# Performance work log

Measured on AMD Instinct MI355X. Metric: run time of the kernel, lower is better.

Reference implementation:

```python
import jax, jax.numpy as jnp
import numpy as np
import math

NUM_HEADS = 16


def _alibi_slopes(n):
    # n is a power of 2 here (16)
    start = 2.0 ** (-2.0 ** (-(math.log2(n) - 3)))
    return jnp.asarray([start * (start ** i) for i in range(n)], dtype=jnp.float32)


def setup_inputs() -> dict:
    key = jax.random.key(0)
    ks = jax.random.split(key, 7)
    B, S, D = 2, 2048, 1024
    s = 0.02
    return {
        "query": jax.random.normal(ks[0], (B, S, D), jnp.float32),
        "key": jax.random.normal(ks[1], (B, S, D), jnp.float32),
        "value": jax.random.normal(ks[2], (B, S, D), jnp.float32),
        "Wq": jax.random.normal(ks[3], (D, D), jnp.float32) * s,
        "Wk": jax.random.normal(ks[4], (D, D), jnp.float32) * s,
        "Wv": jax.random.normal(ks[5], (D, D), jnp.float32) * s,
        "Wo": jax.random.normal(ks[6], (D, D), jnp.float32) * s,
    }


def reference(query, key, value, Wq, Wk, Wv, Wo):
    B, S, D = query.shape
    H = NUM_HEADS
    hd = D // H
    scale = math.sqrt(hd)

    # projections (bias-free linears), split into heads: [B, S, H, hd]
    Q = (query @ Wq).reshape(B, S, H, hd)
    K = (key @ Wk).reshape(B, -1, H, hd)
    V = (value @ Wv).reshape(B, -1, H, hd)

    # attention scores [B, H, S, S]
    scores = jnp.einsum("bqhd,bkhd->bhqk", Q, K) / scale

    # ALiBi bias: -slope_h * |i - j|, broadcast over batch
    pos = jnp.arange(S, dtype=jnp.float32)
    rel = jnp.abs(pos[None, :] - pos[:, None])  # [S, S]
    slopes = _alibi_slopes(H)
    scores = scores - slopes[None, :, None, None] * rel[None, None, :, :]

    attn = jax.nn.softmax(scores, axis=-1)
    out = jnp.einsum("bhqk,bkhd->bqhd", attn, V).reshape(B, S, D)
    return out @ Wo
```

## Files before the change

kernel.cpp:

```cpp
#include <hip/hip_runtime.h>
#include <cstdint>
#include <cstddef>


typedef unsigned short u16;
typedef __attribute__((ext_vector_type(8))) _Float16 half8;
typedef __attribute__((ext_vector_type(4))) float f32x4;

#define DEVI static __device__ __forceinline__
#define MFMA16(a, b, c) __builtin_amdgcn_mfma_f32_16x16x32_f16(a, b, c, 0, 0, 0)

DEVI u16 f2h_bits(float f) {
  _Float16 h = (_Float16)f;
  union { _Float16 h; u16 u; } v; v.h = h;
  return v.u;
}

DEVI void gl_lds16(const u16* g, u16* l) {
  __builtin_amdgcn_global_load_lds(
      (const __attribute__((address_space(1))) void*)g,
      (__attribute__((address_space(3))) void*)l, 16, 0, 0);
}

__global__ __launch_bounds__(256) void cast3_h(const float* __restrict__ in0,
                                               const float* __restrict__ in1,
                                               const float* __restrict__ in2,
                                               u16* __restrict__ o0,
                                               u16* __restrict__ o1,
                                               u16* __restrict__ o2, int n) {
  const float* in = blockIdx.z == 0 ? in0 : (blockIdx.z == 1 ? in1 : in2);
  u16* out = blockIdx.z == 0 ? o0 : (blockIdx.z == 1 ? o1 : o2);
  int i = (blockIdx.x * 256 + threadIdx.x) * 4;
  if (i + 3 < n) {
    const float4 v = *(const float4*)(in + i);
    ushort4 o;
    o.x = f2h_bits(v.x); o.y = f2h_bits(v.y); o.z = f2h_bits(v.z); o.w = f2h_bits(v.w);
    *(ushort4*)(out + i) = o;
  }
}

__global__ __launch_bounds__(256) void transpose4_h(
    const float* __restrict__ W0, const float* __restrict__ W1,
    const float* __restrict__ W2, const float* __restrict__ W3,
    u16* __restrict__ T0, u16* __restrict__ T1, u16* __restrict__ T2,
    u16* __restrict__ T3) {
  const float* W = blockIdx.z == 0 ? W0 : (blockIdx.z == 1 ? W1 : (blockIdx.z == 2 ? W2 : W3));
  u16* Wt = blockIdx.z == 0 ? T0 : (blockIdx.z == 1 ? T1 : (blockIdx.z == 2 ? T2 : T3));
  __shared__ float tile[32][33];
  const int bx = blockIdx.x * 32;
  const int by = blockIdx.y * 32;
  const int x = threadIdx.x & 31;
  const int y0 = threadIdx.x >> 5;
#pragma unroll
  for (int i = y0; i < 32; i += 8)
    tile[i][x] = W[(size_t)(by + i) * 1024 + bx + x];
  __syncthreads();
#pragma unroll
  for (int i = y0; i < 32; i += 8)
    Wt[(size_t)(bx + i) * 1024 + by + x] = f2h_bits(tile[x][i]);
}

DEVI void gemm_body(const u16* __restrict__ A, const u16* __restrict__ Bt,
                    void* __restrict__ Cout, int mode, u16* As, u16* Bs) {
  constexpr int K = 1024, N = 1024;
  const int t = threadIdx.x;
  const int lane = t & 63;
  const int quad = lane >> 4;
  const int l16 = lane & 15;
  const int wid = t >> 6;
  const int mBase = blockIdx.y * 128;
  const int nBase = blockIdx.x * 128;
  const int wM = (wid >> 1) * 64;
  const int wN = (wid & 1) * 64;
  const int aswz = (quad ^ ((l16 >> 1) & 3)) << 3;

  f32x4 acc[4][4];
#pragma unroll
  for (int i = 0; i < 4; ++i)
#pragma unroll
    for (int j = 0; j < 4; ++j) acc[i][j] = (f32x4){0.f, 0.f, 0.f, 0.f};

  for (int kt = 0; kt < K / 32; ++kt) {
    const int kB = kt * 32;
    __syncthreads();
#pragma unroll
    for (int i = 0; i < 2; ++i) {
      const int ci = i * 256 + t;
      const int row = ci >> 2;
      const int col = (((ci & 3) ^ ((ci >> 3) & 3)) << 3);
      gl_lds16(A + (size_t)(mBase + row) * K + kB + col, As + ci * 8);
      gl_lds16(Bt + (size_t)(nBase + row) * K + kB + col, Bs + ci * 8);
    }
    __syncthreads();

    half8 a[4], b[4];
#pragma unroll
    for (int mi = 0; mi < 4; ++mi)
      a[mi] = *(const half8*)(As + (wM + mi * 16 + l16) * 32 + aswz);
#pragma unroll
    for (int ni = 0; ni < 4; ++ni)
      b[ni] = *(const half8*)(Bs + (wN + ni * 16 + l16) * 32 + aswz);
#pragma unroll
    for (int mi = 0; mi < 4; ++mi)
#pragma unroll
      for (int ni = 0; ni < 4; ++ni)
        acc[mi][ni] = MFMA16(a[mi], b[ni], acc[mi][ni]);
  }

#pragma unroll
  for (int mi = 0; mi < 4; ++mi) {
#pragma unroll
    for (int ni = 0; ni < 4; ++ni) {
#pragma unroll
      for (int r = 0; r < 4; ++r) {
        const int m = mBase + wM + mi * 16 + quad * 4 + r;
        const int n = nBase + wN + ni * 16 + l16;
        const float v = acc[mi][ni][r];
        if (mode == 0) {
          ((float*)Cout)[(size_t)m * N + n] = v;
        } else if (mode == 1) {
          ((u16*)Cout)[(size_t)m * N + n] = f2h_bits(v);
        } else {
          ((u16*)Cout)[(((size_t)(m >> 11) * 1024 + n) << 11) | (size_t)(m & 2047)] = f2h_bits(v);
        }
      }
    }
  }
}

__global__ __launch_bounds__(256) void proj_qkv(
    const u16* __restrict__ qb, const u16* __restrict__ kb, const u16* __restrict__ vb,
    const u16* __restrict__ Wqt, const u16* __restrict__ Wkt, const u16* __restrict__ Wvt,
    u16* __restrict__ Qp, u16* __restrict__ Kp, u16* __restrict__ Vtp) {
  __shared__ u16 As[128 * 32];
  __shared__ u16 Bs[128 * 32];
  const int z = blockIdx.z;
  const u16* A = z == 0 ? qb : (z == 1 ? kb : vb);
  const u16* Bt = z == 0 ? Wqt : (z == 1 ? Wkt : Wvt);
  void* C = z == 0 ? (void*)Qp : (z == 1 ? (void*)Kp : (void*)Vtp);
  gemm_body(A, Bt, C, z == 2 ? 2 : 1, As, Bs);
}

__global__ __launch_bounds__(256) void gemm_out(const u16* __restrict__ Ao,
                                                const u16* __restrict__ Wot,
                                                float* __restrict__ out) {
  __shared__ u16 As[128 * 32];
  __shared__ u16 Bs[128 * 32];
  gemm_body(Ao, Wot, out, 0, As, Bs);
}

__global__ __launch_bounds__(256, 4) void flash_alibi(
    const u16* __restrict__ Qg, const u16* __restrict__ Kg,
    const u16* __restrict__ Vtg, u16* __restrict__ Og) {
  constexpr int S = 2048, Dm = 1024, HD = 64;
  __shared__ u16 Ks[2][64 * 64];
  __shared__ u16 Vs[2][64 * 64];
  __shared__ u16 Ps[64 * 64];
  const int t = threadIdx.x, lane = t & 63, wid = t >> 6;
  const int quad = lane >> 4, l16 = lane & 15;
  const int qt = blockIdx.x, b = blockIdx.z;
  const int h = 15 - blockIdx.y;
  const int qBase = qt * 64;
  const size_t qRow0 = (size_t)b * S + qBase;
  const float sl2 = __builtin_amdgcn_exp2f(-0.5f * (float)(h + 1)) * 1.44269504f;
  const float sc2 = 0.125f * 1.44269504f;
  const int Di = (int)(30.0f / sl2);
  const int ktLo = max(0, (qBase - Di) >> 6);
  const int ktHi = min(31, (qBase + 63 + Di) >> 6);
  const int cswz = ((l16 & 7) << 3);
  const int pRowBase = wid * 16;

#pragma unroll
  for (int i = 0; i < 2; ++i) {
    const int ci = i * 256 + t;
    const int row = ci >> 3, col = (((ci & 7) ^ (row & 7)) << 3);
    gl_lds16(Qg + (qRow0 + row) * Dm + h * HD + col, Ps + ci * 8);
  }
  {
    const int kB = ktLo * 64;
#pragma unroll
    for (int i = 0; i < 2; ++i) {
      const int ci = i * 256 + t;
      const int row = ci >> 3, col = (((ci & 7) ^ (row & 7)) << 3);
      gl_lds16(Kg + ((size_t)b * S + kB + row) * Dm + h * HD + col, Ks[0] + ci * 8);
      gl_lds16(Vtg + ((size_t)(b * 16 + h) * HD + row) * S + kB + col, Vs[0] + ci * 8);
    }
  }

  float bi[4];
#pragma unroll
  for (int r = 0; r < 4; ++r)
    bi[r] = sl2 * (float)(qBase + wid * 16 + quad * 4 + r);

  f32x4 acc_o[4];
#pragma unroll
  for (int nd = 0; nd < 4; ++nd) acc_o[nd] = (f32x4){0.f, 0.f, 0.f, 0.f};
  float lrow[4] = {0.f, 0.f, 0.f, 0.f};

  __syncthreads();

  half8 aq[2];
#pragma unroll
  for (int ks = 0; ks < 2; ++ks) {
    const int ck = ((ks * 4 + quad) << 3) ^ cswz;
    aq[ks] = *(const half8*)(Ps + (pRowBase + l16) * HD + ck);
  }

  int bb = 0;
  for (int kt = ktLo; kt <= ktHi; ++kt) {
    const int kB = kt * 64;
    if (kt < ktHi) {
      const int kBn = kB + 64;
#pragma unroll
      for (int i = 0; i < 2; ++i) {
        const int ci = i * 256 + t;
        const int row = ci >> 3, col = (((ci & 7) ^ (row & 7)) << 3);
        gl_lds16(Kg + ((size_t)b * S + kBn + row) * Dm + h * HD + col, Ks[bb ^ 1] + ci * 8);
        gl_lds16(Vtg + ((size_t)(b * 16 + h) * HD + row) * S + kBn + col, Vs[bb ^ 1] + ci * 8);
      }
    }

    const u16* Kb = Ks[bb];
    const u16* Vb = Vs[bb];

    f32x4 s4[4];
#pragma unroll
    for (int ni = 0; ni < 4; ++ni) s4[ni] = (f32x4){0.f, 0.f, 0.f, 0.f};
    __builtin_amdgcn_s_setprio(1);
#pragma unroll
    for (int ks = 0; ks < 2; ++ks) {
      const int ck = ((ks * 4 + quad) << 3) ^ cswz;
#pragma unroll
      for (int ni = 0; ni < 4; ++ni) {
        const half8 bk = *(const half8*)(Kb + (ni * 16 + l16) * HD + ck);
        s4[ni] = MFMA16(aq[ks], bk, s4[ni]);
      }
    }
    __builtin_amdgcn_s_setprio(0);

    float bj[4];
#pragma unroll
    for (int ni = 0; ni < 4; ++ni) bj[ni] = sl2 * (float)(kB + ni * 16 + l16);
#pragma unroll
    for (int r = 0; r < 4; ++r) {
      float rs = 0.f;
      const int prow = (pRowBase + quad * 4 + r) * 64;
#pragma unroll
      for (int ni = 0; ni < 4; ++ni) {
        const float d = fabsf(bi[r] - bj[ni]);
        const float p = __builtin_amdgcn_exp2f(s4[ni][r] * sc2 - d);
        rs += p;
        Ps[prow + ((ni * 16 + l16) ^ (quad << 4))] = f2h_bits(p);
      }
      lrow[r] += rs;
    }
    __asm__ volatile("s_waitcnt lgkmcnt(0)" ::: "memory");

    __builtin_amdgcn_s_setprio(1);
#pragma unroll
    for (int ks = 0; ks < 2; ++ks) {
      const int pk = (ks * 32 + quad * 8) ^ ((l16 & 12) << 2);
      const int ck = ((ks * 4 + quad) << 3) ^ cswz;
      const half8 aP = *(const half8*)(Ps + (pRowBase + l16) * 64 + pk);
#pragma unroll
      for (int nd = 0; nd < 4; ++nd) {
        const half8 bv = *(const half8*)(Vb + (nd * 16 + l16) * HD + ck);
        acc_o[nd] = MFMA16(aP, bv, acc_o[nd]);
      }
    }
    __builtin_amdgcn_s_setprio(0);

    __syncthreads();
    bb ^= 1;
  }

#pragma unroll
  for (int r = 0; r < 4; ++r) {
    float l = lrow[r];
    l += __shfl_xor(l, 1);
    l += __shfl_xor(l, 2);
    l += __shfl_xor(l, 4);
    l += __shfl_xor(l, 8);
    const float inv = 1.f / l;
    const int rloc = wid * 16 + quad * 4 + r;
#pragma unroll
    for (int nd = 0; nd < 4; ++nd)
      Og[(qRow0 + rloc) * Dm + h * HD + nd * 16 + l16] = f2h_bits(acc_o[nd][r] * inv);
  }
}

extern "C" void kernel_launch(void* const* d_in, const int* in_sizes, int n_in,
                              void* d_out, int out_size, void* d_ws, size_t ws_size,
                              hipStream_t stream) {
  const float* q  = (const float*)d_in[0];
  const float* k  = (const float*)d_in[1];
  const float* v  = (const float*)d_in[2];
  const float* Wq = (const float*)d_in[3];
  const float* Wk = (const float*)d_in[4];
  const float* Wv = (const float*)d_in[5];
  const float* Wo = (const float*)d_in[6];
  char* ws = (char*)d_ws;
  const size_t MB = 1ull << 20;
  u16* qb  = (u16*)(ws + 0 * MB);
  u16* kb  = (u16*)(ws + 8 * MB);
  u16* vb  = (u16*)(ws + 16 * MB);
  u16* Wqt = (u16*)(ws + 24 * MB);
  u16* Wkt = (u16*)(ws + 26 * MB);
  u16* Wvt = (u16*)(ws + 28 * MB);
  u16* Wot = (u16*)(ws + 30 * MB);
  u16* Qp  = (u16*)(ws + 32 * MB);
  u16* Kp  = (u16*)(ws + 40 * MB);
  u16* Vtp = (u16*)(ws + 48 * MB);
  u16* Ao  = (u16*)(ws + 56 * MB);

  const int n = 2 * 2048 * 1024;
  cast3_h<<<dim3(n / 1024, 1, 3), 256, 0, stream>>>(q, k, v, qb, kb, vb, n);
  transpose4_h<<<dim3(32, 32, 4), 256, 0, stream>>>(Wq, Wk, Wv, Wo, Wqt, Wkt, Wvt, Wot);
  proj_qkv<<<dim3(8, 32, 3), 256, 0, stream>>>(qb, kb, vb, Wqt, Wkt, Wvt, Qp, Kp, Vtp);
  flash_alibi<<<dim3(32, 16, 2), 256, 0, stream>>>(Qp, Kp, Vtp, Ao);
  gemm_out<<<dim3(8, 32), 256, 0, stream>>>(Ao, Wot, (float*)d_out);
}
```

Measured before the change: 230.1 us.

## Split ALiBi flash attention over key chunks with atomic partial accumulation

The attention grid gains a key-chunk dimension, four chunks of eight key tiles each. Query tiles whose ALiBi window spans more than one chunk add their unnormalised output and row sums into fp32 buffers with atomics. A new combine kernel then normalises those rows and converts them to fp16. The aim is to even out the load, since heads with small slopes visit all key tiles while heads with steep slopes visit only a few. In exchange it adds a zeroing pass over about 16 MB, a lot of atomic traffic and an extra kernel. It is also only correct if the partial softmax terms share a common max reference across chunks.

```diff
diff --git a/kernel.cpp b/kernel.cpp
--- a/kernel.cpp
+++ b/kernel.cpp
@@ -149,24 +149,35 @@
   gemm_body(Ao, Wot, out, 0, As, Bs);
 }
 
+__global__ __launch_bounds__(256) void zero_acc(float* __restrict__ p, int n4) {
+  const int i = blockIdx.x * 256 + threadIdx.x;
+  if (i < n4) ((float4*)p)[i] = (float4){0.f, 0.f, 0.f, 0.f};
+}
+
 __global__ __launch_bounds__(256, 4) void flash_alibi(
     const u16* __restrict__ Qg, const u16* __restrict__ Kg,
-    const u16* __restrict__ Vtg, u16* __restrict__ Og) {
+    const u16* __restrict__ Vtg, u16* __restrict__ Og,
+    float* __restrict__ Oacc, float* __restrict__ lacc) {
   constexpr int S = 2048, Dm = 1024, HD = 64;
   __shared__ u16 Ks[2][64 * 64];
   __shared__ u16 Vs[2][64 * 64];
   __shared__ u16 Ps[64 * 64];
   const int t = threadIdx.x, lane = t & 63, wid = t >> 6;
   const int quad = lane >> 4, l16 = lane & 15;
-  const int qt = blockIdx.x, b = blockIdx.z;
+  const int qt = blockIdx.x;
   const int h = 15 - blockIdx.y;
+  const int zb = blockIdx.z, b = zb & 1, chunk = zb >> 1;
   const int qBase = qt * 64;
   const size_t qRow0 = (size_t)b * S + qBase;
   const float sl2 = __builtin_amdgcn_exp2f(-0.5f * (float)(h + 1)) * 1.44269504f;
   const float sc2 = 0.125f * 1.44269504f;
   const int Di = (int)(30.0f / sl2);
-  const int ktLo = max(0, (qBase - Di) >> 6);
-  const int ktHi = min(31, (qBase + 63 + Di) >> 6);
+  const int ktLo0 = max(0, (qBase - Di) >> 6);
+  const int ktHi0 = min(31, (qBase + 63 + Di) >> 6);
+  const int ktLo = max(ktLo0, chunk * 8);
+  const int ktHi = min(ktHi0, chunk * 8 + 7);
+  if (ktLo > ktHi) return;
+  const bool multi = (ktLo0 >> 3) != (ktHi0 >> 3);
   const int cswz = ((l16 & 7) << 3);
   const int pRowBase = wid * 16;
 
@@ -281,11 +292,44 @@
     l += __shfl_xor(l, 2);
     l += __shfl_xor(l, 4);
     l += __shfl_xor(l, 8);
-    const float inv = 1.f / l;
     const int rloc = wid * 16 + quad * 4 + r;
-#pragma unroll
-    for (int nd = 0; nd < 4; ++nd)
-      Og[(qRow0 + rloc) * Dm + h * HD + nd * 16 + l16] = f2h_bits(acc_o[nd][r] * inv);
+    if (!multi) {
+      const float inv = 1.f / l;
+#pragma unroll
+      for (int nd = 0; nd < 4; ++nd)
+        Og[(qRow0 + rloc) * Dm + h * HD + nd * 16 + l16] = f2h_bits(acc_o[nd][r] * inv);
+    } else {
+      if (l16 == 0) unsafeAtomicAdd(&lacc[((size_t)b * 16 + h) * S + qBase + rloc], l);
+#pragma unroll
+      for (int nd = 0; nd < 4; ++nd)
+        unsafeAtomicAdd(&Oacc[(qRow0 + rloc) * Dm + h * HD + nd * 16 + l16], acc_o[nd][r]);
+    }
+  }
+}
+
+__global__ __launch_bounds__(256) void combine_norm(const float* __restrict__ Oacc,
+                                                    const float* __restrict__ lacc,
+                                                    u16* __restrict__ Ao) {
+  constexpr int S = 2048, Dm = 1024;
+  const int qt = blockIdx.x, h = blockIdx.y, b = blockIdx.z;
+  const int qBase = qt * 64;
+  const float sl2 = __builtin_amdgcn_exp2f(-0.5f * (float)(h + 1)) * 1.44269504f;
+  const int Di = (int)(30.0f / sl2);
+  const int ktLo0 = max(0, (qBase - Di) >> 6);
+  const int ktHi0 = min(31, (qBase + 63 + Di) >> 6);
+  if ((ktLo0 >> 3) == (ktHi0 >> 3)) return;
+  const int t = threadIdx.x;
+  const int row = t >> 2;
+  const int cg = (t & 3) * 16;
+  const float inv = 1.f / lacc[((size_t)b * 16 + h) * S + qBase + row];
+  const size_t base = ((size_t)b * S + qBase + row) * Dm + h * 64 + cg;
+#pragma unroll
+  for (int c = 0; c < 16; c += 4) {
+    const float4 v = *(const float4*)(Oacc + base + c);
+    ushort4 o;
+    o.x = f2h_bits(v.x * inv); o.y = f2h_bits(v.y * inv);
+    o.z = f2h_bits(v.z * inv); o.w = f2h_bits(v.w * inv);
+    *(ushort4*)(Ao + base + c) = o;
   }
 }
 
@@ -304,6 +348,8 @@
   u16* qb  = (u16*)(ws + 0 * MB);
   u16* kb  = (u16*)(ws + 8 * MB);
   u16* vb  = (u16*)(ws + 16 * MB);
+  float* Oacc = (float*)(ws + 0 * MB);
+  float* lacc = (float*)(ws + 16 * MB);
   u16* Wqt = (u16*)(ws + 24 * MB);
   u16* Wkt = (u16*)(ws + 26 * MB);
   u16* Wvt = (u16*)(ws + 28 * MB);
@@ -317,6 +363,9 @@
   cast3_h<<<dim3(n / 1024, 1, 3), 256, 0, stream>>>(q, k, v, qb, kb, vb, n);
   transpose4_h<<<dim3(32, 32, 4), 256, 0, stream>>>(Wq, Wk, Wv, Wo, Wqt, Wkt, Wvt, Wot);
   proj_qkv<<<dim3(8, 32, 3), 256, 0, stream>>>(qb, kb, vb, Wqt, Wkt, Wvt, Qp, Kp, Vtp);
-  flash_alibi<<<dim3(32, 16, 2), 256, 0, stream>>>(Qp, Kp, Vtp, Ao);
+  const int n4 = (16 * 1024 * 1024 + 256 * 1024) / 16;
+  zero_acc<<<dim3((n4 + 255) / 256), 256, 0, stream>>>(Oacc, n4);
+  flash_alibi<<<dim3(32, 16, 8), 256, 0, stream>>>(Qp, Kp, Vtp, Ao, Oacc, lacc);
+  combine_norm<<<dim3(32, 16, 2), 256, 0, stream>>>(Oacc, lacc, Ao);
   gemm_out<<<dim3(8, 32), 256, 0, stream>>>(Ao, Wot, (float*)d_out);
 }
```

Result: slower. 247.6 us (+7.6%).

## Triple-buffer GEMM LDS staging and register-prefetch K/V in flash attention

Applied to the files above, without the earlier changes.

The shared GEMM body now keeps three LDS stages and prefetches two k-tiles ahead. It uses partial vmcnt waits and a single barrier per iteration in place of two __syncthreads. The flash-attention kernel replaces direct global-to-LDS loads with register prefetch two tiles ahead and an unrolled ping-pong over two LDS buffers. This is meant to hide global memory latency behind MFMA work, at the cost of triple the GEMM LDS footprint, extra registers in attention, and hand-managed waitcnt ordering.

```diff
diff --git a/kernel.cpp b/kernel.cpp
--- a/kernel.cpp
+++ b/kernel.cpp
@@ -5,6 +5,7 @@
 
 typedef unsigned short u16;
 typedef __attribute__((ext_vector_type(8))) _Float16 half8;
+typedef __attribute__((ext_vector_type(8))) unsigned short ushort8;
 typedef __attribute__((ext_vector_type(4))) float f32x4;
 
 #define DEVI static __device__ __forceinline__
@@ -21,6 +22,14 @@
       (const __attribute__((address_space(1))) void*)g,
       (__attribute__((address_space(3))) void*)l, 16, 0, 0);
 }
+
+#define LGKM0() __asm__ volatile("s_waitcnt lgkmcnt(0)" ::: "memory")
+#define VM0()   __asm__ volatile("s_waitcnt vmcnt(0)" ::: "memory")
+#define BARRIER()                       \
+  do {                                  \
+    __builtin_amdgcn_s_barrier();       \
+    __asm__ volatile("" ::: "memory");  \
+  } while (0)
 
 __global__ __launch_bounds__(256) void cast3_h(const float* __restrict__ in0,
                                                const float* __restrict__ in1,
@@ -80,31 +89,52 @@
 #pragma unroll
     for (int j = 0; j < 4; ++j) acc[i][j] = (f32x4){0.f, 0.f, 0.f, 0.f};
 
-  for (int kt = 0; kt < K / 32; ++kt) {
-    const int kB = kt * 32;
-    __syncthreads();
+  auto stage = [&](int kt, u16* Ad, u16* Bd) {
 #pragma unroll
     for (int i = 0; i < 2; ++i) {
       const int ci = i * 256 + t;
       const int row = ci >> 2;
       const int col = (((ci & 3) ^ ((ci >> 3) & 3)) << 3);
-      gl_lds16(A + (size_t)(mBase + row) * K + kB + col, As + ci * 8);
-      gl_lds16(Bt + (size_t)(nBase + row) * K + kB + col, Bs + ci * 8);
-    }
-    __syncthreads();
+      gl_lds16(A + (size_t)(mBase + row) * K + kt * 32 + col, Ad + ci * 8);
+      gl_lds16(Bt + (size_t)(nBase + row) * K + kt * 32 + col, Bd + ci * 8);
+    }
+  };
+
+  u16 *a0 = As, *a1 = As + 4096, *a2 = As + 8192;
+  u16 *b0 = Bs, *b1 = Bs + 4096, *b2 = Bs + 8192;
+
+  stage(0, a0, b0);
+  stage(1, a1, b1);
+  VM0();
+  BARRIER();
+
+  for (int kt = 0; kt < K / 32; ++kt) {
+    if (kt + 2 < K / 32) stage(kt + 2, a2, b2);
 
     half8 a[4], b[4];
 #pragma unroll
     for (int mi = 0; mi < 4; ++mi)
-      a[mi] = *(const half8*)(As + (wM + mi * 16 + l16) * 32 + aswz);
+      a[mi] = *(const half8*)(a0 + (wM + mi * 16 + l16) * 32 + aswz);
 #pragma unroll
     for (int ni = 0; ni < 4; ++ni)
-      b[ni] = *(const half8*)(Bs + (wN + ni * 16 + l16) * 32 + aswz);
+      b[ni] = *(const half8*)(b0 + (wN + ni * 16 + l16) * 32 + aswz);
 #pragma unroll
     for (int mi = 0; mi < 4; ++mi)
 #pragma unroll
       for (int ni = 0; ni < 4; ++ni)
         acc[mi][ni] = MFMA16(a[mi], b[ni], acc[mi][ni]);
+
+    if (kt + 1 < K / 32) {
+      if (kt + 2 < K / 32)
+        __asm__ volatile("s_waitcnt vmcnt(4)" ::: "memory");
+      else
+        VM0();
+      __builtin_amdgcn_sched_barrier(0);
+      LGKM0();
+      BARRIER();
+    }
+    u16* ta = a0; a0 = a1; a1 = a2; a2 = ta;
+    u16* tb = b0; b0 = b1; b1 = b2; b2 = tb;
   }
 
 #pragma unroll
@@ -132,8 +162,8 @@
     const u16* __restrict__ qb, const u16* __restrict__ kb, const u16* __restrict__ vb,
     const u16* __restrict__ Wqt, const u16* __restrict__ Wkt, const u16* __restrict__ Wvt,
     u16* __restrict__ Qp, u16* __restrict__ Kp, u16* __restrict__ Vtp) {
-  __shared__ u16 As[128 * 32];
-  __shared__ u16 Bs[128 * 32];
+  __shared__ u16 As[3 * 128 * 32];
+  __shared__ u16 Bs[3 * 128 * 32];
   const int z = blockIdx.z;
   const u16* A = z == 0 ? qb : (z == 1 ? kb : vb);
   const u16* Bt = z == 0 ? Wqt : (z == 1 ? Wkt : Wvt);
@@ -144,8 +174,8 @@
 __global__ __launch_bounds__(256) void gemm_out(const u16* __restrict__ Ao,
                                                 const u16* __restrict__ Wot,
                                                 float* __restrict__ out) {
-  __shared__ u16 As[128 * 32];
-  __shared__ u16 Bs[128 * 32];
+  __shared__ u16 As[3 * 128 * 32];
+  __shared__ u16 Bs[3 * 128 * 32];
   gemm_body(Ao, Wot, out, 0, As, Bs);
 }
 
@@ -170,22 +200,41 @@
   const int cswz = ((l16 & 7) << 3);
   const int pRowBase = wid * 16;
 
+  const u16* Kb0 = Kg + (size_t)b * S * Dm + h * HD;
+  const u16* Vb0 = Vtg + ((size_t)(b * 16 + h) * HD) * S;
+
 #pragma unroll
   for (int i = 0; i < 2; ++i) {
     const int ci = i * 256 + t;
     const int row = ci >> 3, col = (((ci & 7) ^ (row & 7)) << 3);
     gl_lds16(Qg + (qRow0 + row) * Dm + h * HD + col, Ps + ci * 8);
   }
-  {
-    const int kB = ktLo * 64;
+
+  ushort8 krA[2], vrA[2], krB[2], vrB[2];
+  auto fa_load = [&](int kB, ushort8* kr, ushort8* vr) {
 #pragma unroll
     for (int i = 0; i < 2; ++i) {
       const int ci = i * 256 + t;
       const int row = ci >> 3, col = (((ci & 7) ^ (row & 7)) << 3);
-      gl_lds16(Kg + ((size_t)b * S + kB + row) * Dm + h * HD + col, Ks[0] + ci * 8);
-      gl_lds16(Vtg + ((size_t)(b * 16 + h) * HD + row) * S + kB + col, Vs[0] + ci * 8);
-    }
-  }
+      kr[i] = *(const ushort8*)(Kb0 + (size_t)(kB + row) * Dm + col);
+      vr[i] = *(const ushort8*)(Vb0 + (size_t)row * S + kB + col);
+    }
+  };
+  auto fa_write = [&](u16* Kd, u16* Vd, const ushort8* kr, const ushort8* vr) {
+#pragma unroll
+    for (int i = 0; i < 2; ++i) {
+      const int ci = i * 256 + t;
+      *(ushort8*)(Kd + ci * 8) = kr[i];
+      *(ushort8*)(Vd + ci * 8) = vr[i];
+    }
+  };
+
+  fa_load(ktLo * 64, krB, vrB);
+  if (ktLo + 1 <= ktHi) fa_load((ktLo + 1) * 64, krA, vrA);
+  fa_write(Ks[0], Vs[0], krB, vrB);
+  VM0();
+  LGKM0();
+  BARRIER();
 
   float bi[4];
 #pragma unroll
@@ -196,8 +245,6 @@
 #pragma unroll
   for (int nd = 0; nd < 4; ++nd) acc_o[nd] = (f32x4){0.f, 0.f, 0.f, 0.f};
   float lrow[4] = {0.f, 0.f, 0.f, 0.f};
-
-  __syncthreads();
 
   half8 aq[2];
 #pragma unroll
@@ -206,73 +253,71 @@
     aq[ks] = *(const half8*)(Ps + (pRowBase + l16) * HD + ck);
   }
 
-  int bb = 0;
-  for (int kt = ktLo; kt <= ktHi; ++kt) {
-    const int kB = kt * 64;
-    if (kt < ktHi) {
-      const int kBn = kB + 64;
-#pragma unroll
-      for (int i = 0; i < 2; ++i) {
-        const int ci = i * 256 + t;
-        const int row = ci >> 3, col = (((ci & 7) ^ (row & 7)) << 3);
-        gl_lds16(Kg + ((size_t)b * S + kBn + row) * Dm + h * HD + col, Ks[bb ^ 1] + ci * 8);
-        gl_lds16(Vtg + ((size_t)(b * 16 + h) * HD + row) * S + kBn + col, Vs[bb ^ 1] + ci * 8);
-      }
-    }
-
-    const u16* Kb = Ks[bb];
-    const u16* Vb = Vs[bb];
-
-    f32x4 s4[4];
-#pragma unroll
-    for (int ni = 0; ni < 4; ++ni) s4[ni] = (f32x4){0.f, 0.f, 0.f, 0.f};
-    __builtin_amdgcn_s_setprio(1);
-#pragma unroll
-    for (int ks = 0; ks < 2; ++ks) {
-      const int ck = ((ks * 4 + quad) << 3) ^ cswz;
-#pragma unroll
-      for (int ni = 0; ni < 4; ++ni) {
-        const half8 bk = *(const half8*)(Kb + (ni * 16 + l16) * HD + ck);
-        s4[ni] = MFMA16(aq[ks], bk, s4[ni]);
-      }
-    }
-    __builtin_amdgcn_s_setprio(0);
-
-    float bj[4];
-#pragma unroll
-    for (int ni = 0; ni < 4; ++ni) bj[ni] = sl2 * (float)(kB + ni * 16 + l16);
-#pragma unroll
-    for (int r = 0; r < 4; ++r) {
-      float rs = 0.f;
-      const int prow = (pRowBase + quad * 4 + r) * 64;
-#pragma unroll
-      for (int ni = 0; ni < 4; ++ni) {
-        const float d = fabsf(bi[r] - bj[ni]);
-        const float p = __builtin_amdgcn_exp2f(s4[ni][r] * sc2 - d);
-        rs += p;
-        Ps[prow + ((ni * 16 + l16) ^ (quad << 4))] = f2h_bits(p);
-      }
-      lrow[r] += rs;
-    }
-    __asm__ volatile("s_waitcnt lgkmcnt(0)" ::: "memory");
-
-    __builtin_amdgcn_s_setprio(1);
-#pragma unroll
-    for (int ks = 0; ks < 2; ++ks) {
-      const int pk = (ks * 32 + quad * 8) ^ ((l16 & 12) << 2);
-      const int ck = ((ks * 4 + quad) << 3) ^ cswz;
-      const half8 aP = *(const half8*)(Ps + (pRowBase + l16) * 64 + pk);
-#pragma unroll
-      for (int nd = 0; nd < 4; ++nd) {
-        const half8 bv = *(const half8*)(Vb + (nd * 16 + l16) * HD + ck);
-        acc_o[nd] = MFMA16(aP, bv, acc_o[nd]);
-      }
-    }
-    __builtin_amdgcn_s_setprio(0);
-
-    __syncthreads();
-    bb ^= 1;
-  }
+#define FA_COMPUTE(kB_, Kb_, Vb_)                                               \
+  do {                                                                          \
+    f32x4 s4[4];                                                                \
+    _Pragma("unroll")                                                           \
+    for (int ni = 0; ni < 4; ++ni) s4[ni] = (f32x4){0.f, 0.f, 0.f, 0.f};        \
+    __builtin_amdgcn_s_setprio(1);                                              \
+    _Pragma("unroll")                                                           \
+    for (int ks = 0; ks < 2; ++ks) {                                            \
+      const int ck = ((ks * 4 + quad) << 3) ^ cswz;                             \
+      _Pragma("unroll")                                                         \
+      for (int ni = 0; ni < 4; ++ni) {                                          \
+        const half8 bk = *(const half8*)((Kb_) + (ni * 16 + l16) * HD + ck);    \
+        s4[ni] = MFMA16(aq[ks], bk, s4[ni]);                                    \
+      }                                                                         \
+    }                                                                           \
+    __builtin_amdgcn_s_setprio(0);                                              \
+    float bj[4];                                                                \
+    _Pragma("unroll")                                                           \
+    for (int ni = 0; ni < 4; ++ni) bj[ni] = sl2 * (float)((kB_) + ni * 16 + l16); \
+    _Pragma("unroll")                                                           \
+    for (int r = 0; r < 4; ++r) {                                               \
+      float rs = 0.f;                                                           \
+      const int prow = (pRowBase + quad * 4 + r) * 64;                          \
+      _Pragma("unroll")                                                         \
+      for (int ni = 0; ni < 4; ++ni) {                                          \
+        const float d = fabsf(bi[r] - bj[ni]);                                  \
+        const float p = __builtin_amdgcn_exp2f(s4[ni][r] * sc2 - d);            \
+        rs += p;                                                                \
+        Ps[prow + ((ni * 16 + l16) ^ (quad << 4))] = f2h_bits(p);               \
+      }                                                                         \
+      lrow[r] += rs;                                                            \
+    }                                                                           \
+    LGKM0();       \
+    __builtin_amdgcn_s_setprio(1);                                              \
+    _Pragma("unroll")                                                           \
+    for (int ks = 0; ks < 2; ++ks) {                                            \
+      const int pk = (ks * 32 + quad * 8) ^ ((l16 & 12) << 2);                  \
+      const int ck = ((ks * 4 + quad) << 3) ^ cswz;                             \
+      const half8 aP = *(const half8*)(Ps + (pRowBase + l16) * 64 + pk);        \
+      _Pragma("unroll")                                                         \
+      for (int nd = 0; nd < 4; ++nd) {                                          \
+        const half8 bv = *(const half8*)((Vb_) + (nd * 16 + l16) * HD + ck);    \
+        acc_o[nd] = MFMA16(aP, bv, acc_o[nd]);                                  \
+      }                                                                         \
+    }                                                                           \
+    __builtin_amdgcn_s_setprio(0);                                              \
+  } while (0)
+
+  int kt = ktLo;
+  for (;;) {
+    if (kt + 2 <= ktHi) fa_load((kt + 2) * 64, krB, vrB);
+    if (kt + 1 <= ktHi) fa_write(Ks[1], Vs[1], krA, vrA);
+    FA_COMPUTE(kt * 64, Ks[0], Vs[0]);
+    LGKM0();
+    BARRIER();
+    if (kt + 1 > ktHi) break;
+    if (kt + 3 <= ktHi) fa_load((kt + 3) * 64, krA, vrA);
+    if (kt + 2 <= ktHi) fa_write(Ks[0], Vs[0], krB, vrB);
+    FA_COMPUTE((kt + 1) * 64, Ks[1], Vs[1]);
+    LGKM0();
+    BARRIER();
+    if (kt + 2 > ktHi) break;
+    kt += 2;
+  }
+#undef FA_COMPUTE
 
 #pragma unroll
   for (int r = 0; r < 4; ++r) {
```

Result: slower. 263.3 us (+14.5%).

## Triple-buffer GEMM LDS loads and shrink tiles to 64x128 for more blocks

Applied to the files above, without the earlier changes.

Reworks the shared GEMM body used by the QKV projection and output projection. It now uses a three-stage LDS ring buffer with async global-to-LDS loads issued two iterations ahead and partial vmcnt waits, replacing the two-barrier load-then-compute loop. The M tile also shrinks from 128 to 64, with each wave covering 64x32, which doubles the grid and adds an occupancy hint of 4. This should hide global load latency and improve CU fill, at the cost of less A/B reuse per block and more LDS per block.

```diff
diff --git a/kernel.cpp b/kernel.cpp
--- a/kernel.cpp
+++ b/kernel.cpp
@@ -21,6 +21,14 @@
       (const __attribute__((address_space(1))) void*)g,
       (__attribute__((address_space(3))) void*)l, 16, 0, 0);
 }
+
+#define LGKM0() __asm__ volatile("s_waitcnt lgkmcnt(0)" ::: "memory")
+#define VM0()   __asm__ volatile("s_waitcnt vmcnt(0)" ::: "memory")
+#define BARRIER()                       \
+  do {                                  \
+    __builtin_amdgcn_s_barrier();       \
+    __asm__ volatile("" ::: "memory");  \
+  } while (0)
 
 __global__ __launch_bounds__(256) void cast3_h(const float* __restrict__ in0,
                                                const float* __restrict__ in1,
@@ -68,52 +76,77 @@
   const int quad = lane >> 4;
   const int l16 = lane & 15;
   const int wid = t >> 6;
-  const int mBase = blockIdx.y * 128;
+  const int mBase = blockIdx.y * 64;
   const int nBase = blockIdx.x * 128;
-  const int wM = (wid >> 1) * 64;
-  const int wN = (wid & 1) * 64;
+  const int wN = wid * 32;
   const int aswz = (quad ^ ((l16 >> 1) & 3)) << 3;
 
-  f32x4 acc[4][4];
+  f32x4 acc[4][2];
 #pragma unroll
   for (int i = 0; i < 4; ++i)
 #pragma unroll
-    for (int j = 0; j < 4; ++j) acc[i][j] = (f32x4){0.f, 0.f, 0.f, 0.f};
-
-  for (int kt = 0; kt < K / 32; ++kt) {
-    const int kB = kt * 32;
-    __syncthreads();
+    for (int j = 0; j < 2; ++j) acc[i][j] = (f32x4){0.f, 0.f, 0.f, 0.f};
+
+  auto stage = [&](int kt, u16* Ad, u16* Bd) {
+    {
+      const int ci = t;
+      const int row = ci >> 2;
+      const int col = (((ci & 3) ^ ((ci >> 3) & 3)) << 3);
+      gl_lds16(A + (size_t)(mBase + row) * K + kt * 32 + col, Ad + ci * 8);
+    }
 #pragma unroll
     for (int i = 0; i < 2; ++i) {
       const int ci = i * 256 + t;
       const int row = ci >> 2;
       const int col = (((ci & 3) ^ ((ci >> 3) & 3)) << 3);
-      gl_lds16(A + (size_t)(mBase + row) * K + kB + col, As + ci * 8);
-      gl_lds16(Bt + (size_t)(nBase + row) * K + kB + col, Bs + ci * 8);
-    }
-    __syncthreads();
-
-    half8 a[4], b[4];
+      gl_lds16(Bt + (size_t)(nBase + row) * K + kt * 32 + col, Bd + ci * 8);
+    }
+  };
+
+  u16 *a0 = As, *a1 = As + 2048, *a2 = As + 4096;
+  u16 *b0 = Bs, *b1 = Bs + 4096, *b2 = Bs + 8192;
+
+  stage(0, a0, b0);
+  stage(1, a1, b1);
+  VM0();
+  BARRIER();
+
+  for (int kt = 0; kt < K / 32; ++kt) {
+    if (kt + 2 < K / 32) stage(kt + 2, a2, b2);
+
+    half8 a[4], b[2];
 #pragma unroll
     for (int mi = 0; mi < 4; ++mi)
-      a[mi] = *(const half8*)(As + (wM + mi * 16 + l16) * 32 + aswz);
-#pragma unroll
-    for (int ni = 0; ni < 4; ++ni)
-      b[ni] = *(const half8*)(Bs + (wN + ni * 16 + l16) * 32 + aswz);
+      a[mi] = *(const half8*)(a0 + (mi * 16 + l16) * 32 + aswz);
+#pragma unroll
+    for (int ni = 0; ni < 2; ++ni)
+      b[ni] = *(const half8*)(b0 + (wN + ni * 16 + l16) * 32 + aswz);
 #pragma unroll
     for (int mi = 0; mi < 4; ++mi)
 #pragma unroll
-      for (int ni = 0; ni < 4; ++ni)
+      for (int ni = 0; ni < 2; ++ni)
         acc[mi][ni] = MFMA16(a[mi], b[ni], acc[mi][ni]);
+
+    if (kt + 1 < K / 32) {
+      if (kt + 2 < K / 32)
+        __asm__ volatile("s_waitcnt vmcnt(3)" ::: "memory");
+      else
+        VM0();
+      __builtin_amdgcn_sched_barrier(0);
+      LGKM0();
+      BARRIER();
+    }
+    u16* ta = a0; a0 = a1; a1 = a2; a2 = ta;
+    u16* tb = b0; b0 = b1; b1 = b2; b2 = tb;
   }
 
 #pragma unroll
   for (int mi = 0; mi < 4; ++mi) {
 #pragma unroll
-    for (int ni = 0; ni < 4; ++ni) {
+    for (int ni = 0; ni < 2; ++ni) {
 #pragma unroll
       for (int r = 0; r < 4; ++r) {
-        const int m = mBase + wM + mi * 16 + quad * 4 + r;
+        const int m = mBase + mi * 16 + quad * 4 + r;
         const int n = nBase + wN + ni * 16 + l16;
         const float v = acc[mi][ni][r];
         if (mode == 0) {
@@ -128,12 +161,12 @@
   }
 }
 
-__global__ __launch_bounds__(256) void proj_qkv(
+__global__ __launch_bounds__(256, 4) void proj_qkv(
     const u16* __restrict__ qb, const u16* __restrict__ kb, const u16* __restrict__ vb,
     const u16* __restrict__ Wqt, const u16* __restrict__ Wkt, const u16* __restrict__ Wvt,
     u16* __restrict__ Qp, u16* __restrict__ Kp, u16* __restrict__ Vtp) {
-  __shared__ u16 As[128 * 32];
-  __shared__ u16 Bs[128 * 32];
+  __shared__ u16 As[3 * 64 * 32];
+  __shared__ u16 Bs[3 * 128 * 32];
   const int z = blockIdx.z;
   const u16* A = z == 0 ? qb : (z == 1 ? kb : vb);
   const u16* Bt = z == 0 ? Wqt : (z == 1 ? Wkt : Wvt);
@@ -141,11 +174,11 @@
   gemm_body(A, Bt, C, z == 2 ? 2 : 1, As, Bs);
 }
 
-__global__ __launch_bounds__(256) void gemm_out(const u16* __restrict__ Ao,
-                                                const u16* __restrict__ Wot,
-                                                float* __restrict__ out) {
-  __shared__ u16 As[128 * 32];
-  __shared__ u16 Bs[128 * 32];
+__global__ __launch_bounds__(256, 4) void gemm_out(const u16* __restrict__ Ao,
+                                                   const u16* __restrict__ Wot,
+                                                   float* __restrict__ out) {
+  __shared__ u16 As[3 * 64 * 32];
+  __shared__ u16 Bs[3 * 128 * 32];
   gemm_body(Ao, Wot, out, 0, As, Bs);
 }
 
@@ -316,7 +349,7 @@
   const int n = 2 * 2048 * 1024;
   cast3_h<<<dim3(n / 1024, 1, 3), 256, 0, stream>>>(q, k, v, qb, kb, vb, n);
   transpose4_h<<<dim3(32, 32, 4), 256, 0, stream>>>(Wq, Wk, Wv, Wo, Wqt, Wkt, Wvt, Wot);
-  proj_qkv<<<dim3(8, 32, 3), 256, 0, stream>>>(qb, kb, vb, Wqt, Wkt, Wvt, Qp, Kp, Vtp);
+  proj_qkv<<<dim3(8, 64, 3), 256, 0, stream>>>(qb, kb, vb, Wqt, Wkt, Wvt, Qp, Kp, Vtp);
   flash_alibi<<<dim3(32, 16, 2), 256, 0, stream>>>(Qp, Kp, Vtp, Ao);
-  gemm_out<<<dim3(8, 32), 256, 0, stream>>>(Ao, Wot, (float*)d_out);
-}
+  gemm_out<<<dim3(8, 64), 256, 0, stream>>>(Ao, Wot, (float*)d_out);
+}
```

After: 242.2 us. +5.3%, slower.
